# Kernel tuning notes

Hardware: AMD Instinct MI355X
Metric: run time of the kernel (lower is better)

The kernel has to match this reference:

```python
import jax, jax.numpy as jnp
import numpy as np

# model dims
B_, S_, D_ = 2, 2048, 1024
D_STATE, EXPAND, HEADDIM, CHUNK, NGROUPS = 128, 2, 64, 64, 1
D_INNER = EXPAND * D_
NHEADS = D_INNER // HEADDIM  # 32 ssd heads
D_PROJ = 2 * D_INNER + 2 * NGROUPS * D_STATE + NHEADS  # 4384
H_, KV_, HD_ = 16, 4, 64  # attention heads / kv heads / head dim
ROPE_DIMS = 16
MLP_DIM = int(3.0 * D_)


def _rmsnorm(x, w=None, eps=1e-5):
    y = x * jax.lax.rsqrt(jnp.mean(x * x, axis=-1, keepdims=True) + eps)
    return y * w if w is not None else y


def _layernorm(x, w, b, eps=1e-5):
    m = jnp.mean(x, axis=-1, keepdims=True)
    v = jnp.mean((x - m) ** 2, axis=-1, keepdims=True)
    return (x - m) * jax.lax.rsqrt(v + eps) * w + b


def _segsum(x):
    # (..., T) -> (..., T, T) lower-tri cumulative sums, -inf above diag
    T = x.shape[-1]
    i = jnp.arange(T)
    xx = jnp.where(i[:, None] > i[None, :], jnp.broadcast_to(x[..., None], x.shape + (T,)), 0.0)
    s = jnp.cumsum(xx, axis=-2)
    return jnp.where(i[:, None] >= i[None, :], s, -jnp.inf)


def _ssd_chunked(x, A, B, C, chunk):
    # x:(b,s,h,p) A:(b,s,h) B,C:(b,s,g,n)
    b, s, h, p = x.shape
    g, n = B.shape[2], B.shape[3]
    if g < h:
        B = jnp.repeat(B, h // g, axis=2)
        C = jnp.repeat(C, h // g, axis=2)
    c = s // chunk
    x = x.reshape(b, c, chunk, h, p)
    A = A.reshape(b, c, chunk, h).transpose(0, 3, 1, 2)  # b h c l
    B = B.reshape(b, c, chunk, h, n)
    C = C.reshape(b, c, chunk, h, n)
    L = jnp.exp(_segsum(A))
    Y_diag = jnp.einsum('bclhn,bcshn,bhcls,bcshp->bclhp', C, B, L, x)
    A_cum = jnp.cumsum(A, axis=-1)
    decay_states = jnp.exp(A_cum[..., -1:] - A_cum)
    states = jnp.einsum('bclhn,bhcl,bclhp->bchpn', B, decay_states, x)
    decay_chunk = jnp.exp(_segsum(jnp.pad(A_cum[..., -1], ((0, 0), (0, 0), (1, 0)))))
    new_states = jnp.einsum('bhzc,bchpn->bzhpn', decay_chunk[:, :, :c, 1:c + 1], states)
    Y_off = jnp.einsum('bclhn,bchpn,bhcl->bclhp', C, new_states, jnp.exp(A_cum))
    return (Y_diag + Y_off).reshape(b, s, h, p)


def _rope_cos_sin(s, rd, base=10000.0):
    inv = 1.0 / base ** (jnp.arange(0, rd, 2, dtype=jnp.float32) / rd)
    f = jnp.outer(jnp.arange(s, dtype=jnp.float32), inv)  # (s, rd/2)
    return jnp.cos(f)[None, :, None, :], jnp.sin(f)[None, :, None, :]


def _apply_rope(x, cos, sin, rd):
    xr, xp = x[..., :rd], x[..., rd:]
    half = rd // 2
    x1, x2 = xr[..., :half], xr[..., half:]
    xr = jnp.concatenate([x1 * cos + x2 * sin, -x1 * sin + x2 * cos], axis=-1)
    return jnp.concatenate([xr, xp], axis=-1)


def _mamba_block(x, mnorm_w, in_w, out_w, Dp, dt_b, A_log, Bn_w, Cn_w):
    b, s, _ = x.shape
    h = _rmsnorm(x, mnorm_w)
    zxbcdt = h @ in_w.T
    z, xs, Bc, Cc, dt = jnp.split(
        zxbcdt,
        [D_INNER, 2 * D_INNER, 2 * D_INNER + NGROUPS * D_STATE, 2 * D_INNER + 2 * NGROUPS * D_STATE],
        axis=-1)
    dt = jax.nn.softplus(dt + dt_b)  # (b,s,nheads)
    A = -jnp.exp(A_log)  # (nheads,)
    xs = xs.reshape(b, s, NHEADS, HEADDIM)
    Bc = _rmsnorm(Bc.reshape(b, s, NGROUPS, D_STATE), Bn_w)
    Cc = _rmsnorm(Cc.reshape(b, s, NGROUPS, D_STATE), Cn_w)
    y = _ssd_chunked(xs * dt[..., None], A[None, None, :] * dt, Bc, Cc, CHUNK)
    y = y + xs * Dp[None, None, :, None]
    y = y * jax.nn.silu(z).reshape(b, s, NHEADS, HEADDIM)
    return x + y.reshape(b, s, D_INNER) @ out_w.T


def _attn_block(x, ln1_w, ln1_b, cq_w, ck_w, cv_w, cproj_w, q_gain, ln2_w, ln2_b, fc_w, proj_w):
    b, s, d = x.shape
    h = _layernorm(x, ln1_w, ln1_b)
    q = (h @ cq_w.T).reshape(b, s, H_, HD_)
    k = (h @ ck_w.T).reshape(b, s, KV_, HD_)
    v = (h @ cv_w.T).reshape(b, s, KV_, HD_)
    eps = jnp.finfo(x.dtype).eps
    q = _rmsnorm(q, eps=eps)
    k = _rmsnorm(k, eps=eps)
    cos, sin = _rope_cos_sin(s, ROPE_DIMS)
    q = _apply_rope(q, cos, sin, ROPE_DIMS)
    k = _apply_rope(k, cos, sin, ROPE_DIMS)
    q = q * q_gain[None, None, :, None]
    rep = H_ // KV_
    k = jnp.repeat(k, rep, axis=2)
    v = jnp.repeat(v, rep, axis=2)
    scores = jnp.einsum('bqhd,bkhd->bhqk', q, k) / np.float32(np.sqrt(HD_))
    i = jnp.arange(s)
    scores = jnp.where(i[:, None] >= i[None, :], scores, -jnp.inf)
    w = jax.nn.softmax(scores, axis=-1)
    y = jnp.einsum('bhqk,bkhd->bqhd', w, v).reshape(b, s, d)
    x = x + y @ cproj_w.T
    h = _layernorm(x, ln2_w, ln2_b)
    return x + jax.nn.silu(h @ fc_w.T) @ proj_w.T


def setup_inputs() -> dict:
    key = jax.random.key(0)
    ks = jax.random.split(key, 16)
    rn = lambda k, shp, sc=0.02: (jax.random.normal(k, shp, dtype=jnp.float32) * sc)
    return {
        'x': jax.random.normal(ks[0], (B_, S_, D_), dtype=jnp.float32),
        'mnorm_w': jnp.ones((D_,), jnp.float32),
        'in_proj_w': rn(ks[1], (D_PROJ, D_)),
        'out_proj_w': rn(ks[2], (D_, D_INNER)),
        'D_param': jnp.ones((NHEADS,), jnp.float32),
        'dt_bias': rn(ks[3], (NHEADS,), 0.1),
        'A_log': jnp.log(0.5 + jax.random.uniform(ks[4], (NHEADS,), dtype=jnp.float32) * 0.5),
        'Bn_w': jnp.ones((D_STATE,), jnp.float32),
        'Cn_w': jnp.ones((D_STATE,), jnp.float32),
        'ln1_w': jnp.ones((D_,), jnp.float32),
        'ln1_b': jnp.zeros((D_,), jnp.float32),
        'cq_w': rn(ks[5], (D_, D_)),
        'ck_w': rn(ks[6], (KV_ * HD_, D_)),
        'cv_w': rn(ks[7], (KV_ * HD_, D_)),
        'cproj_w': rn(ks[8], (D_, D_)),
        'q_gain': jnp.full((H_,), 5.25, jnp.float32),
        'ln2_w': jnp.ones((D_,), jnp.float32),
        'ln2_b': jnp.zeros((D_,), jnp.float32),
        'fc_w': rn(ks[9], (MLP_DIM, D_)),
        'proj_w': rn(ks[10], (D_, MLP_DIM)),
    }


def reference(x, mnorm_w, in_proj_w, out_proj_w, D_param, dt_bias, A_log, Bn_w, Cn_w,
              ln1_w, ln1_b, cq_w, ck_w, cv_w, cproj_w, q_gain, ln2_w, ln2_b, fc_w, proj_w):
    x = _mamba_block(x, mnorm_w, in_proj_w, out_proj_w, D_param, dt_bias, A_log, Bn_w, Cn_w)
    x = _attn_block(x, ln1_w, ln1_b, cq_w, ck_w, cv_w, cproj_w, q_gain, ln2_w, ln2_b, fc_w, proj_w)
    return x
```

## Files before the change

kernel.cpp:

```cpp
#include <hip/hip_runtime.h>
#include <hip/hip_bf16.h>
#include <math.h>

#define B_    2
#define S_    2048
#define D_    1024
#define DI    2048
#define NH    32
#define HD    64
#define DS    128
#define CH    64
#define NC    32
#define DP    4384
#define HATT  16
#define KVH   4
#define RD    16
#define MLP   3072
#define ROWS  (B_*S_)

typedef __bf16 bf16;
typedef __bf16 bf16x8 __attribute__((ext_vector_type(8)));
typedef __bf16 bf16x4 __attribute__((ext_vector_type(4)));
typedef float  f32x4  __attribute__((ext_vector_type(4)));

__device__ __forceinline__ void async_copy16(const void* g, void* l) {
  __builtin_amdgcn_global_load_lds(
      (const __attribute__((address_space(1))) unsigned int*)g,
      (__attribute__((address_space(3))) unsigned int*)l, 16, 0, 0);
}

__device__ __forceinline__ float waveReduceSum(float v) {
#pragma unroll
  for (int off = 32; off > 0; off >>= 1) v += __shfl_down(v, off, 64);
  return v;
}

template<int NW>
__device__ __forceinline__ float blockReduceSum(float v, float* sh) {
  v = waveReduceSum(v);
  int lane = threadIdx.x & 63, wid = threadIdx.x >> 6;
  if (lane == 0) sh[wid] = v;
  __syncthreads();
  float s = 0.f;
#pragma unroll
  for (int i = 0; i < NW; i++) s += sh[i];
  __syncthreads();
  return s;
}

struct CastSeg { const float* src; bf16* dst; int nval; int ntot; int blk0; };
struct CastArgs { CastSeg seg[8]; };

__global__ __launch_bounds__(256) void castw_all(CastArgs a) {
  int blk = blockIdx.x;
  int si = 0;
#pragma unroll
  for (int i = 1; i < 8; i++) if (blk >= a.seg[i].blk0) si = i;
  CastSeg s = a.seg[si];
  int i = ((blk - s.blk0) * 256 + threadIdx.x) * 4;
  if (i >= s.ntot) return;
  float4 v = {0.f, 0.f, 0.f, 0.f};
  if (i < s.nval) v = *(const float4*)(s.src + i);
  bf16x4 o;
  o[0] = (bf16)v.x; o[1] = (bf16)v.y; o[2] = (bf16)v.z; o[3] = (bf16)v.w;
  *(bf16x4*)(s.dst + i) = o;
}

__global__ __launch_bounds__(256) void rmsnorm_k(const float* __restrict__ x,
                                                 const float* __restrict__ w,
                                                 bf16* __restrict__ y, int n) {
  __shared__ float sh[4];
  size_t row = blockIdx.x;
  const float* xr = x + row * n;
  bf16* yr = y + row * n;
  float ss = 0.f;
  for (int i = threadIdx.x; i < n; i += 256) { float v = xr[i]; ss += v * v; }
  ss = blockReduceSum<4>(ss, sh);
  float inv = rsqrtf(ss / n + 1e-5f);
  for (int i = threadIdx.x; i < n; i += 256) yr[i] = (bf16)(xr[i] * inv * w[i]);
}

template<int ACT, typename OT>
__global__ __launch_bounds__(256) void gemm_mfma(const bf16* __restrict__ A,
                                                 const bf16* __restrict__ W,
                                                 const float* __restrict__ R,
                                                 OT* __restrict__ C,
                                                 int M, int N, int K) {
  __shared__ bf16 As[128 * 32];
  __shared__ bf16 Ws[128 * 32];
  int tid = threadIdx.x, lane = tid & 63, wave = tid >> 6;
  int mt = M >> 7;
  int bid = blockIdx.x;
  int bm = (bid % mt) * 128, bn = (bid / mt) * 128;
  const bf16* gA0 = A + (size_t)(bm + wave * 32 + (lane >> 2)) * K + (lane & 3) * 8;
  const bf16* gA1 = gA0 + (size_t)16 * K;
  const bf16* gW0 = W + (size_t)(bn + wave * 32 + (lane >> 2)) * K + (lane & 3) * 8;
  const bf16* gW1 = gW0 + (size_t)16 * K;
  bf16* lA0 = As + wave * 32 * 32;
  bf16* lA1 = lA0 + 16 * 32;
  bf16* lW0 = Ws + wave * 32 * 32;
  bf16* lW1 = lW0 + 16 * 32;
  int fr = lane & 15, fq = lane >> 4;
  int wm = wave >> 1, wn = wave & 1;
  const bf16* pA = As + (wm * 64 + fr) * 32 + fq * 8;
  const bf16* pW = Ws + (wn * 64 + fr) * 32 + fq * 8;
  f32x4 acc[4][4] = {};
  for (int k0 = 0; k0 < K; k0 += 32) {
    async_copy16(gA0, lA0);
    async_copy16(gA1, lA1);
    async_copy16(gW0, lW0);
    async_copy16(gW1, lW1);
    gA0 += 32; gA1 += 32; gW0 += 32; gW1 += 32;
    __syncthreads();
    bf16x8 af[4], bfr[4];
#pragma unroll
    for (int mi = 0; mi < 4; mi++) af[mi] = *(const bf16x8*)(pA + mi * 16 * 32);
#pragma unroll
    for (int ni = 0; ni < 4; ni++) bfr[ni] = *(const bf16x8*)(pW + ni * 16 * 32);
#pragma unroll
    for (int mi = 0; mi < 4; mi++)
#pragma unroll
      for (int ni = 0; ni < 4; ni++)
        acc[mi][ni] = __builtin_amdgcn_mfma_f32_16x16x32_bf16(af[mi], bfr[ni], acc[mi][ni], 0, 0, 0);
    __syncthreads();
  }
#pragma unroll
  for (int mi = 0; mi < 4; mi++) {
    int row = bm + wm * 64 + mi * 16 + fq * 4;
#pragma unroll
    for (int ni = 0; ni < 4; ni++) {
      int col = bn + wn * 64 + ni * 16 + fr;
      if (col < N) {
#pragma unroll
        for (int r = 0; r < 4; r++) {
          float v = acc[mi][ni][r];
          if (ACT == 1) v = v / (1.f + __expf(-v));
          if (R) v += R[(size_t)(row + r) * N + col];
          C[(size_t)(row + r) * N + col] = (OT)v;
        }
      }
    }
  }
}

__global__ __launch_bounds__(256) void gemm_sk(const bf16* __restrict__ A,
                                               const bf16* __restrict__ W,
                                               bf16* __restrict__ P,
                                               int M, int N, int K, int kchunk) {
  __shared__ bf16 As[128 * 32];
  __shared__ bf16 Ws[128 * 32];
  int tid = threadIdx.x, lane = tid & 63, wave = tid >> 6;
  int mt = M >> 7;
  int bid = blockIdx.x;
  int bm = (bid % mt) * 128, bn = (bid / mt) * 128;
  int ks = blockIdx.z;
  int kbeg = ks * kchunk;
  const bf16* gA0 = A + (size_t)(bm + wave * 32 + (lane >> 2)) * K + kbeg + (lane & 3) * 8;
  const bf16* gA1 = gA0 + (size_t)16 * K;
  const bf16* gW0 = W + (size_t)(bn + wave * 32 + (lane >> 2)) * K + kbeg + (lane & 3) * 8;
  const bf16* gW1 = gW0 + (size_t)16 * K;
  bf16* lA0 = As + wave * 32 * 32;
  bf16* lA1 = lA0 + 16 * 32;
  bf16* lW0 = Ws + wave * 32 * 32;
  bf16* lW1 = lW0 + 16 * 32;
  int fr = lane & 15, fq = lane >> 4;
  int wm = wave >> 1, wn = wave & 1;
  const bf16* pA = As + (wm * 64 + fr) * 32 + fq * 8;
  const bf16* pW = Ws + (wn * 64 + fr) * 32 + fq * 8;
  f32x4 acc[4][4] = {};
  for (int k0 = 0; k0 < kchunk; k0 += 32) {
    async_copy16(gA0, lA0);
    async_copy16(gA1, lA1);
    async_copy16(gW0, lW0);
    async_copy16(gW1, lW1);
    gA0 += 32; gA1 += 32; gW0 += 32; gW1 += 32;
    __syncthreads();
    bf16x8 af[4], bfr[4];
#pragma unroll
    for (int mi = 0; mi < 4; mi++) af[mi] = *(const bf16x8*)(pA + mi * 16 * 32);
#pragma unroll
    for (int ni = 0; ni < 4; ni++) bfr[ni] = *(const bf16x8*)(pW + ni * 16 * 32);
#pragma unroll
    for (int mi = 0; mi < 4; mi++)
#pragma unroll
      for (int ni = 0; ni < 4; ni++)
        acc[mi][ni] = __builtin_amdgcn_mfma_f32_16x16x32_bf16(af[mi], bfr[ni], acc[mi][ni], 0, 0, 0);
    __syncthreads();
  }
  bf16* Pp = P + (size_t)ks * M * N;
#pragma unroll
  for (int mi = 0; mi < 4; mi++) {
    int row = bm + wm * 64 + mi * 16 + fq * 4;
#pragma unroll
    for (int ni = 0; ni < 4; ni++) {
      int col = bn + wn * 64 + ni * 16 + fr;
#pragma unroll
      for (int r = 0; r < 4; r++)
        Pp[(size_t)(row + r) * N + col] = (bf16)acc[mi][ni][r];
    }
  }
}

__global__ __launch_bounds__(256) void reduce_ln2(const bf16* __restrict__ p0,
                                                  const bf16* __restrict__ p1,
                                                  const float* __restrict__ res,
                                                  const float* __restrict__ w,
                                                  const float* __restrict__ b,
                                                  float* __restrict__ xo,
                                                  bf16* __restrict__ ho) {
  __shared__ float sh[4];
  size_t o = (size_t)blockIdx.x * 1024;
  int i = threadIdx.x * 4;
  bf16x4 a = *(const bf16x4*)(p0 + o + i);
  bf16x4 c = *(const bf16x4*)(p1 + o + i);
  f32x4 rv = *(const f32x4*)(res + o + i);
  f32x4 v;
  float s = 0.f, s2 = 0.f;
#pragma unroll
  for (int j = 0; j < 4; j++) {
    v[j] = (float)a[j] + (float)c[j] + rv[j];
    s += v[j]; s2 += v[j] * v[j];
  }
  s  = blockReduceSum<4>(s,  sh);
  s2 = blockReduceSum<4>(s2, sh);
  float mean = s / 1024.f;
  float var  = s2 / 1024.f - mean * mean;
  float inv  = rsqrtf(var + 1e-5f);
  f32x4 wv = *(const f32x4*)(w + i);
  f32x4 bv = *(const f32x4*)(b + i);
  *(f32x4*)(xo + o + i) = v;
  bf16x4 hv;
#pragma unroll
  for (int j = 0; j < 4; j++) hv[j] = (bf16)((v[j] - mean) * inv * wv[j] + bv[j]);
  *(bf16x4*)(ho + o + i) = hv;
}

__global__ __launch_bounds__(256) void reduce_out3(const bf16* __restrict__ p0,
                                                   const bf16* __restrict__ p1,
                                                   const bf16* __restrict__ p2,
                                                   const float* __restrict__ res,
                                                   float* __restrict__ out) {
  int i = (blockIdx.x * 256 + threadIdx.x) * 4;
  bf16x4 a = *(const bf16x4*)(p0 + i);
  bf16x4 c = *(const bf16x4*)(p1 + i);
  bf16x4 d = *(const bf16x4*)(p2 + i);
  f32x4 v = *(const f32x4*)(res + i);
#pragma unroll
  for (int j = 0; j < 4; j++) v[j] += (float)a[j] + (float)c[j] + (float)d[j];
  *(f32x4*)(out + i) = v;
}

__global__ __launch_bounds__(256) void reduce_qkv(const bf16* __restrict__ P,
                                                  const float* __restrict__ q_gain,
                                                  bf16* __restrict__ q,
                                                  bf16* __restrict__ k,
                                                  bf16* __restrict__ v) {
  __shared__ float buf[1536];
  size_t row = blockIdx.x;
  size_t o = row * 1536;
  const bf16* p0 = P + o;
  const bf16* p1 = P + (size_t)ROWS * 1536 + o;
  int tid = threadIdx.x;
  for (int i = tid; i < 384; i += 256) {
    bf16x4 a = *(const bf16x4*)(p0 + i * 4);
    bf16x4 c = *(const bf16x4*)(p1 + i * 4);
    f32x4 vv;
#pragma unroll
    for (int j = 0; j < 4; j++) vv[j] = (float)a[j] + (float)c[j];
    *(f32x4*)(buf + i * 4) = vv;
  }
  __syncthreads();
  int lane = tid & 63, w = tid >> 6;
  int s = (int)(row & (S_ - 1));
  int ri = lane & 7;
  float rinv = __expf(-(float)ri * (0.125f * 9.210340371976184f));
  float ang = (float)s * rinv;
  float cs = cosf(ang), sn = sinf(ang);
#pragma unroll
  for (int j = 0; j < 6; j++) {
    int hh = w * 6 + j;
    float val = buf[hh * 64 + lane];
    if (hh < 20) {
      float ss = val * val;
#pragma unroll
      for (int off = 32; off > 0; off >>= 1) ss += __shfl_xor(ss, off, 64);
      val *= rsqrtf(ss / 64.f + 1.1920929e-7f);
      float other = __shfl_xor(val, 8, 64);
      float res = val;
      if (lane < RD) res = (lane < 8) ? (val * cs + other * sn) : (val * cs - other * sn);
      if (hh < 16) {
        res *= q_gain[hh];
        q[row * (HATT * HD) + hh * HD + lane] = (bf16)res;
      } else {
        k[row * (KVH * HD) + (hh - 16) * HD + lane] = (bf16)res;
      }
    } else {
      v[row * (KVH * HD) + (hh - 20) * HD + lane] = (bf16)val;
    }
  }
}

__global__ __launch_bounds__(512, 2) void gemm256_inproj(const bf16* __restrict__ A,
                                                         const bf16* __restrict__ W,
                                                         bf16* __restrict__ zt,
                                                         bf16* __restrict__ xt,
                                                         bf16* __restrict__ bcdt) {
  __shared__ bf16 lds[3 * 16384];
  int tid = threadIdx.x;
  int lane = tid & 63, w = tid >> 6;
  int fr = lane & 15, fq = lane >> 4;
  int rdswz = (fq ^ (fr & 3)) * 8;
  int sswz = (lane & 3) ^ ((lane >> 2) & 3);
  int bid = blockIdx.x;
  if (bid < 256) {
    int sb = (bid & 7) * 32 + (bid >> 3);
    int bm = (sb & 15) * 256;
    int bn = (sb >> 4) * 256;
    int wm = w >> 2, wn = w & 3;
    int srow = w * 32 + (lane >> 2);
    const bf16* gA = A + (size_t)(bm + srow) * 1024 + sswz * 8;
    const bf16* gW = W + (size_t)(bn + srow) * 1024 + sswz * 8;
    int sbase = w * 1024;
    f32x4 acc[8][4] = {};
    {
      bf16* bA = lds + sbase;
      bf16* bB = lds + 8192 + sbase;
      async_copy16(gA, bA);
      async_copy16(gA + 16 * 1024, bA + 512);
      async_copy16(gW, bB);
      async_copy16(gW + 16 * 1024, bB + 512);
    }
    int cur = 0, nxt = 1;
    for (int t = 0; t < 32; t++) {
      if (t + 1 < 32) {
        const bf16* ga = gA + (t + 1) * 32;
        const bf16* gw = gW + (t + 1) * 32;
        bf16* bA = lds + nxt * 16384 + sbase;
        bf16* bB = lds + nxt * 16384 + 8192 + sbase;
        async_copy16(ga, bA);
        async_copy16(ga + 16 * 1024, bA + 512);
        async_copy16(gw, bB);
        async_copy16(gw + 16 * 1024, bB + 512);
        asm volatile("s_waitcnt vmcnt(4)" ::: "memory");
      } else {
        asm volatile("s_waitcnt vmcnt(0)" ::: "memory");
      }
      __builtin_amdgcn_sched_barrier(0);
      __builtin_amdgcn_s_barrier();
      __builtin_amdgcn_sched_barrier(0);
      const bf16* cA = lds + cur * 16384;
      const bf16* cB = cA + 8192;
      bf16x8 af[8], bfv[4];
#pragma unroll
      for (int mi = 0; mi < 8; mi++)
        af[mi] = *(const bf16x8*)(cA + (wm * 128 + mi * 16 + fr) * 32 + rdswz);
#pragma unroll
      for (int ni = 0; ni < 4; ni++)
        bfv[ni] = *(const bf16x8*)(cB + (wn * 64 + ni * 16 + fr) * 32 + rdswz);
      __builtin_amdgcn_s_setprio(1);
#pragma unroll
      for (int mi = 0; mi < 8; mi++)
#pragma unroll
        for (int ni = 0; ni < 4; ni++)
          acc[mi][ni] = __builtin_amdgcn_mfma_f32_16x16x32_bf16(af[mi], bfv[ni], acc[mi][ni], 0, 0, 0);
      __builtin_amdgcn_s_setprio(0);
      cur = nxt; nxt = nxt + 1; if (nxt == 3) nxt = 0;
    }
    bf16* base = (bn < 2048) ? zt : xt;
    int bq = bm >> 11, bmS = bm & 2047;
    bf16* Ts = lds;
#pragma unroll 1
    for (int g = 0; g < 4; g++) {
      __syncthreads();
      if (wn == g) {
#pragma unroll
        for (int mi = 0; mi < 8; mi++)
#pragma unroll
          for (int ni = 0; ni < 4; ni++) {
            bf16x4 o;
#pragma unroll
            for (int r = 0; r < 4; r++) o[r] = (bf16)acc[mi][ni][r];
            *(bf16x4*)(Ts + (ni * 16 + fr) * 264 + wm * 128 + mi * 16 + fq * 4) = o;
          }
      }
      __syncthreads();
      int hh = ((bn & 2047) + g * 64) >> 6;
      bf16* dst = base + ((size_t)(bq * NH + hh) * HD) * S_ + bmS;
#pragma unroll
      for (int i = 0; i < 4; i++) {
        int idx = tid + i * 512;
        int p = idx >> 5, sc = (idx & 31) * 8;
        *(bf16x8*)(dst + (size_t)p * S_ + sc) = *(const bf16x8*)(Ts + p * 264 + sc);
      }
    }
  } else {
    int lb = bid - 256;
    int bm = (lb & 31) * 128;
    int bn = 4096 + (lb >> 5) * 128;
    int wm = w >> 1, wn = w & 1;
    int srow = w * 16 + (lane >> 2);
    const bf16* gA = A + (size_t)(bm + srow) * 1024 + sswz * 8;
    const bf16* gW = W + (size_t)(bn + srow) * 1024 + sswz * 8;
    int sbase = w * 512;
    f32x4 acc[2][4] = {};
    {
      async_copy16(gA, lds + sbase);
      async_copy16(gW, lds + 4096 + sbase);
    }
    int cur = 0, nxt = 1;
    for (int t = 0; t < 32; t++) {
      if (t + 1 < 32) {
        const bf16* ga = gA + (t + 1) * 32;
        const bf16* gw = gW + (t + 1) * 32;
        async_copy16(ga, lds + nxt * 8192 + sbase);
        async_copy16(gw, lds + nxt * 8192 + 4096 + sbase);
        asm volatile("s_waitcnt vmcnt(2)" ::: "memory");
      } else {
        asm volatile("s_waitcnt vmcnt(0)" ::: "memory");
      }
      __builtin_amdgcn_sched_barrier(0);
      __builtin_amdgcn_s_barrier();
      __builtin_amdgcn_sched_barrier(0);
      const bf16* cA = lds + cur * 8192;
      const bf16* cB = cA + 4096;
      bf16x8 af[2], bfv[4];
#pragma unroll
      for (int mi = 0; mi < 2; mi++)
        af[mi] = *(const bf16x8*)(cA + (wm * 32 + mi * 16 + fr) * 32 + rdswz);
#pragma unroll
      for (int ni = 0; ni < 4; ni++)
        bfv[ni] = *(const bf16x8*)(cB + (wn * 64 + ni * 16 + fr) * 32 + rdswz);
#pragma unroll
      for (int mi = 0; mi < 2; mi++)
#pragma unroll
        for (int ni = 0; ni < 4; ni++)
          acc[mi][ni] = __builtin_amdgcn_mfma_f32_16x16x32_bf16(af[mi], bfv[ni], acc[mi][ni], 0, 0, 0);
      cur = nxt; nxt = nxt + 1; if (nxt == 3) nxt = 0;
    }
#pragma unroll
    for (int mi = 0; mi < 2; mi++) {
      int row = bm + wm * 32 + mi * 16 + fq * 4;
#pragma unroll
      for (int ni = 0; ni < 4; ni++) {
        int col = bn + wn * 64 + ni * 16 + fr;
        if (col < 4384) {
#pragma unroll
          for (int r = 0; r < 4; r++)
            bcdt[(size_t)(row + r) * 288 + (col - 4096)] = (bf16)acc[mi][ni][r];
        }
      }
    }
  }
}

__global__ __launch_bounds__(256) void t64(const bf16* __restrict__ in, bf16* __restrict__ out,
                                           int istr, size_t io, size_t oo, int n_nt) {
  __shared__ bf16 T[64 * 72];
  int bid = blockIdx.x;
  int st = bid & 31;
  int nt = (bid >> 5) % n_nt;
  int outer = bid / (32 * n_nt);
  const bf16* ip = in + outer * io + (size_t)st * 64 * istr + nt * 64;
  int tid = threadIdx.x;
#pragma unroll
  for (int i = 0; i < 2; i++) {
    int cid = tid + i * 256; int s = cid >> 3, pc = (cid & 7) * 8;
    *(bf16x8*)(T + s * 72 + pc) = *(const bf16x8*)(ip + (size_t)s * istr + pc);
  }
  __syncthreads();
  bf16* op = out + outer * oo + (size_t)nt * 64 * 2048 + st * 64;
#pragma unroll
  for (int i = 0; i < 2; i++) {
    int cid = tid + i * 256; int p = cid >> 3, sc = (cid & 7) * 8;
    bf16x8 o;
#pragma unroll
    for (int j = 0; j < 8; j++) o[j] = T[(sc + j) * 72 + p];
    *(bf16x8*)(op + (size_t)p * 2048 + sc) = o;
  }
}

__global__ __launch_bounds__(64) void ssd_prep(const bf16* __restrict__ bcdt,
                                               const float* __restrict__ dt_bias,
                                               const float* __restrict__ A_log,
                                               float* __restrict__ dt_c,
                                               float* __restrict__ ddc,
                                               float* __restrict__ ac_c,
                                               float* __restrict__ T_out) {
  int bid = blockIdx.x;
  int c = bid % NC, hh = (bid / NC) % NH, b = bid / (NC * NH);
  int l = threadIdx.x;
  size_t row = (size_t)b * S_ + c * 64 + l;
  float raw = (float)bcdt[row * 288 + 256 + hh] + dt_bias[hh];
  float dtv = (raw > 20.f) ? raw : log1pf(__expf(raw));
  float a = -__expf(A_log[hh]) * dtv;
  float ps = a;
#pragma unroll
  for (int off = 1; off < 64; off <<= 1) {
    float t = __shfl_up(ps, off, 64);
    if (l >= off) ps += t;
  }
  float a63 = __shfl(ps, 63, 64);
  size_t o = ((size_t)b * NH + hh) * S_ + c * 64 + l;
  dt_c[o] = dtv;
  ac_c[o] = ps;
  ddc[o] = __expf(a63 - ps) * dtv;
  if (l == 63) T_out[(b * NH + hh) * NC + c] = ps;
}

__global__ __launch_bounds__(128) void bc_norm(const bf16* __restrict__ bcdt,
                                               const float* __restrict__ Bw,
                                               const float* __restrict__ Cw,
                                               bf16* __restrict__ Bn,
                                               bf16* __restrict__ Cn) {
  __shared__ float shb[2], shc[2];
  size_t row = blockIdx.x;
  int i = threadIdx.x;
  float bv = (float)bcdt[row * 288 + i];
  float cv = (float)bcdt[row * 288 + 128 + i];
  float sb = waveReduceSum(bv * bv);
  float sc = waveReduceSum(cv * cv);
  int lane = threadIdx.x & 63, wid = threadIdx.x >> 6;
  if (lane == 0) { shb[wid] = sb; shc[wid] = sc; }
  __syncthreads();
  float tb = shb[0] + shb[1];
  float tc = shc[0] + shc[1];
  Bn[row * DS + i] = (bf16)(bv * rsqrtf(tb / DS + 1e-5f) * Bw[i]);
  Cn[row * DS + i] = (bf16)(cv * rsqrtf(tc / DS + 1e-5f) * Cw[i]);
}

__global__ __launch_bounds__(256) void ssd_states(const bf16* __restrict__ Xt,
                                                  const bf16* __restrict__ Btr,
                                                  const float* __restrict__ ddc,
                                                  bf16* __restrict__ states) {
  __shared__ bf16 Xs[64 * 72];
  __shared__ bf16 Bs[128 * 72];
  int bid = blockIdx.x;
  int h = bid % NH;
  int c = (bid / NH) % NC;
  int b = bid / (NH * NC);
  int tid = threadIdx.x, lane = tid & 63, w = tid >> 6;
  int fr = lane & 15, fq = lane >> 4;
  const size_t xbase = (size_t)(b * NH + h) * HD * S_ + c * 64;
  const size_t dbase = (size_t)(b * NH + h) * S_ + c * 64;
#pragma unroll
  for (int i = 0; i < 2; i++) {
    int cid = tid + i * 256; int p = cid >> 3, sc = (cid & 7) * 8;
    bf16x8 xv = *(const bf16x8*)(Xt + xbase + (size_t)p * S_ + sc);
    f32x4 d0 = *(const f32x4*)(ddc + dbase + sc);
    f32x4 d1 = *(const f32x4*)(ddc + dbase + sc + 4);
    bf16x8 o;
#pragma unroll
    for (int j = 0; j < 4; j++) { o[j] = (bf16)((float)xv[j] * d0[j]); o[4 + j] = (bf16)((float)xv[4 + j] * d1[j]); }
    *(bf16x8*)(Xs + p * 72 + sc) = o;
  }
  const size_t bbase = (size_t)b * 128 * S_ + c * 64;
#pragma unroll
  for (int i = 0; i < 4; i++) {
    int cid = tid + i * 256; int n = cid >> 3, sc = (cid & 7) * 8;
    *(bf16x8*)(Bs + n * 72 + sc) = *(const bf16x8*)(Btr + bbase + (size_t)n * S_ + sc);
  }
  __syncthreads();
  f32x4 acc[4][2] = {};
#pragma unroll
  for (int ks = 0; ks < 2; ks++) {
    bf16x8 a[4], bb[2];
#pragma unroll
    for (int pt = 0; pt < 4; pt++) a[pt] = *(const bf16x8*)(Xs + (pt * 16 + fr) * 72 + ks * 32 + fq * 8);
#pragma unroll
    for (int n2 = 0; n2 < 2; n2++) bb[n2] = *(const bf16x8*)(Bs + ((2 * w + n2) * 16 + fr) * 72 + ks * 32 + fq * 8);
#pragma unroll
    for (int pt = 0; pt < 4; pt++)
#pragma unroll
      for (int n2 = 0; n2 < 2; n2++)
        acc[pt][n2] = __builtin_amdgcn_mfma_f32_16x16x32_bf16(a[pt], bb[n2], acc[pt][n2], 0, 0, 0);
  }
  bf16* outp = states + (size_t)bid * 8192;
#pragma unroll
  for (int pt = 0; pt < 4; pt++)
#pragma unroll
    for (int n2 = 0; n2 < 2; n2++) {
      int n = (2 * w + n2) * 16 + fr;
#pragma unroll
      for (int r = 0; r < 4; r++)
        outp[(size_t)(pt * 16 + fq * 4 + r) * 128 + n] = (bf16)acc[pt][n2][r];
    }
}

__global__ __launch_bounds__(256) void ssd_scan(bf16* __restrict__ states,
                                                const float* __restrict__ T) {
  __shared__ float eT[NC];
  int part = blockIdx.x & 7;
  int bh = blockIdx.x >> 3;
  int b = bh / NH, h = bh % NH;
  if (threadIdx.x < NC) eT[threadIdx.x] = __expf(T[(size_t)(b * NH + h) * NC + threadIdx.x]);
  __syncthreads();
  const size_t cstride = (size_t)NH * HD * DS;
  size_t base = ((size_t)b * NC * NH + h) * (HD * DS);
#pragma unroll
  for (int j = 0; j < 4; j++) {
    int e = part * 1024 + threadIdx.x + j * 256;
    float carry = 0.f;
    size_t idx = base + e;
    for (int c = 0; c < NC; c++) {
      float sv = (float)states[idx];
      states[idx] = (bf16)carry;
      carry = sv + eT[c] * carry;
      idx += cstride;
    }
  }
}

__global__ __launch_bounds__(256) void ssd_out(const bf16* __restrict__ Cn,
                                               const bf16* __restrict__ Bn,
                                               const bf16* __restrict__ Xt,
                                               const bf16* __restrict__ Zt,
                                               const float* __restrict__ dt_c,
                                               const float* __restrict__ ac_c,
                                               const bf16* __restrict__ states,
                                               const float* __restrict__ Dp,
                                               bf16* __restrict__ ybf) {
  __shared__ bf16 Cs[64 * 136];
  __shared__ bf16 BNs[64 * 136];
  __shared__ bf16 Xs[64 * 72];
  __shared__ bf16 G[64 * 72];
  __shared__ float acs[64];
  int bid = blockIdx.x;
  int h = bid % NH;
  int c = (bid / NH) % NC;
  int b = bid / (NH * NC);
  int tid = threadIdx.x, lane = tid & 63, w = tid >> 6;
  int fr = lane & 15, fq = lane >> 4;
  size_t row0 = (size_t)b * S_ + c * 64;
  const size_t abase = (size_t)(b * NH + h) * S_ + c * 64;
  if (tid < 64) acs[tid] = ac_c[abase + tid];
#pragma unroll
  for (int i = 0; i < 4; i++) {
    int cid = tid + i * 256; int l = cid >> 4, nc = (cid & 15) * 8;
    float e = __expf(ac_c[abase + l]);
    bf16x8 cv = *(const bf16x8*)(Cn + (row0 + l) * DS + nc);
    bf16x8 o;
#pragma unroll
    for (int j = 0; j < 8; j++) o[j] = (bf16)((float)cv[j] * e);
    *(bf16x8*)(Cs + l * 136 + nc) = o;
    *(bf16x8*)(BNs + l * 136 + nc) = *(const bf16x8*)(Bn + (row0 + l) * DS + nc);
  }
  const size_t xbase = (size_t)(b * NH + h) * HD * S_ + c * 64;
#pragma unroll
  for (int i = 0; i < 2; i++) {
    int cid = tid + i * 256; int p = cid >> 3, sc = (cid & 7) * 8;
    bf16x8 xv = *(const bf16x8*)(Xt + xbase + (size_t)p * S_ + sc);
    f32x4 d0 = *(const f32x4*)(dt_c + abase + sc);
    f32x4 d1 = *(const f32x4*)(dt_c + abase + sc + 4);
    bf16x8 o;
#pragma unroll
    for (int j = 0; j < 4; j++) { o[j] = (bf16)((float)xv[j] * d0[j]); o[4 + j] = (bf16)((float)xv[4 + j] * d1[j]); }
    *(bf16x8*)(Xs + p * 72 + sc) = o;
  }
  __syncthreads();
  bf16x8 ca[4];
#pragma unroll
  for (int ks = 0; ks < 4; ks++) ca[ks] = *(const bf16x8*)(Cs + (w * 16 + fr) * 136 + ks * 32 + fq * 8);
  f32x4 cb[4] = {};
  for (int st = 0; st <= w; st++)
#pragma unroll
    for (int ks = 0; ks < 4; ks++)
      cb[st] = __builtin_amdgcn_mfma_f32_16x16x32_bf16(ca[ks],
                 *(const bf16x8*)(BNs + (st * 16 + fr) * 136 + ks * 32 + fq * 8), cb[st], 0, 0, 0);
#pragma unroll
  for (int st = 0; st < 4; st++) {
    float es = (st <= w) ? __expf(-acs[st * 16 + fr]) : 0.f;
#pragma unroll
    for (int r = 0; r < 4; r++) {
      int lloc = fq * 4 + r;
      float g = 0.f;
      if (st < w) g = cb[st][r] * es;
      else if (st == w) g = (lloc >= fr) ? cb[st][r] * es : 0.f;
      G[(w * 16 + lloc) * 72 + st * 16 + fr] = (bf16)g;
    }
  }
  f32x4 acc[4] = {};
  {
    bf16x8 ga0 = *(const bf16x8*)(G + (w * 16 + fr) * 72 + fq * 8);
    bf16x8 ga1 = *(const bf16x8*)(G + (w * 16 + fr) * 72 + 32 + fq * 8);
#pragma unroll
    for (int pt = 0; pt < 4; pt++) {
      acc[pt] = __builtin_amdgcn_mfma_f32_16x16x32_bf16(ga0,
                  *(const bf16x8*)(Xs + (pt * 16 + fr) * 72 + fq * 8), acc[pt], 0, 0, 0);
      acc[pt] = __builtin_amdgcn_mfma_f32_16x16x32_bf16(ga1,
                  *(const bf16x8*)(Xs + (pt * 16 + fr) * 72 + 32 + fq * 8), acc[pt], 0, 0, 0);
    }
  }
  __syncthreads();
  const bf16* stp = states + (size_t)bid * 8192;
#pragma unroll
  for (int i = 0; i < 4; i++) {
    int cid = tid + i * 256; int p = cid >> 4, nc = (cid & 15) * 8;
    *(bf16x8*)(BNs + p * 136 + nc) = *(const bf16x8*)(stp + (size_t)p * 128 + nc);
  }
  __syncthreads();
#pragma unroll
  for (int pt = 0; pt < 4; pt++)
#pragma unroll
    for (int ks = 0; ks < 4; ks++)
      acc[pt] = __builtin_amdgcn_mfma_f32_16x16x32_bf16(ca[ks],
                  *(const bf16x8*)(BNs + (pt * 16 + fr) * 136 + ks * 32 + fq * 8), acc[pt], 0, 0, 0);
  float dph = Dp[h];
#pragma unroll
  for (int pt = 0; pt < 4; pt++) {
    int p = pt * 16 + fr;
    size_t tb = (xbase + (size_t)p * S_) + w * 16 + fq * 4;
    bf16x4 xs4 = *(const bf16x4*)(Xt + tb);
    bf16x4 z4  = *(const bf16x4*)(Zt + tb);
#pragma unroll
    for (int r = 0; r < 4; r++) {
      int l = w * 16 + fq * 4 + r;
      float yv = acc[pt][r] + (float)xs4[r] * dph;
      float z = (float)z4[r];
      yv *= z / (1.f + __expf(-z));
      ybf[((row0 + l) * NH + h) * HD + p] = (bf16)yv;
    }
  }
}

#define KSTR 72
#define PSTR 72
__global__ __launch_bounds__(256) void attn_mfma(const bf16* __restrict__ q,
                                                 const bf16* __restrict__ k,
                                                 const bf16* __restrict__ vtr,
                                                 bf16* __restrict__ Po,
                                                 float* __restrict__ Ls) {
  __shared__ bf16 Ks[64 * KSTR];
  __shared__ bf16 Vs[64 * KSTR];
  __shared__ bf16 Pl[4][32 * PSTR];
  int c = 39 - blockIdx.x;
  int g = (c < 4) ? 0 : (c < 12) ? 1 : (c < 24) ? 2 : 3;
  int gbase = (g == 0) ? 0 : (g == 1) ? 4 : (g == 2) ? 12 : 24;
  int d = c - gbase;
  int qt = 4 * g + d / (g + 1);
  int sk = d % (g + 1);
  int h = blockIdx.y, b = blockIdx.z;
  int kvh = h >> 2;
  int tid = threadIdx.x, lane = tid & 63, w = tid >> 6;
  int fr = lane & 15, fq = lane >> 4;
  const float SC = 0.18033688011112042f;
  const float M2 = 62.0f;
  int kt0 = sk * 8;
  int ktend = min(kt0 + 8, 2 * qt + 2);
  int qbase = qt * 128 + w * 32;
  int qmaxw = qbase + 31;
  bf16x8 bq[2][2];
#pragma unroll
  for (int qc = 0; qc < 2; qc++)
#pragma unroll
    for (int ks = 0; ks < 2; ks++)
      bq[qc][ks] = *(const bf16x8*)(q + (size_t)(b * S_ + qbase + qc * 16 + fr) * (HATT * HD)
                                      + h * HD + ks * 32 + fq * 8);
  int sr = tid >> 3, sc8 = (tid & 7) * 8;
  const bf16* kg = k + ((size_t)(b * S_) + sr) * (KVH * HD) + kvh * HD + sc8;
  const bf16* vg = vtr + ((size_t)(b * KVH + kvh) * HD + sr) * S_ + sc8;
  bf16x8 krg0, krg1, vrg0, vrg1;
  {
    const bf16* kp = kg + (size_t)kt0 * 64 * (KVH * HD);
    const bf16* vp = vg + (size_t)kt0 * 64;
    krg0 = *(const bf16x8*)(kp);
    krg1 = *(const bf16x8*)(kp + (size_t)32 * (KVH * HD));
    vrg0 = *(const bf16x8*)(vp);
    vrg1 = *(const bf16x8*)(vp + (size_t)32 * S_);
  }
  float lsum[2] = {0.f, 0.f};
  f32x4 yacc[2][4] = {};
  bf16* Plw = Pl[w];
  for (int kt = kt0; kt < ktend; kt++) {
    __syncthreads();
    *(bf16x8*)(&Ks[sr * KSTR + sc8]) = krg0;
    *(bf16x8*)(&Ks[(sr + 32) * KSTR + sc8]) = krg1;
    *(bf16x8*)(&Vs[sr * KSTR + sc8]) = vrg0;
    *(bf16x8*)(&Vs[(sr + 32) * KSTR + sc8]) = vrg1;
    __syncthreads();
    if ((kt + 1) < ktend) {
      const bf16* kp = kg + (size_t)(kt + 1) * 64 * (KVH * HD);
      const bf16* vp = vg + (size_t)(kt + 1) * 64;
      krg0 = *(const bf16x8*)(kp);
      krg1 = *(const bf16x8*)(kp + (size_t)32 * (KVH * HD));
      vrg0 = *(const bf16x8*)(vp);
      vrg1 = *(const bf16x8*)(vp + (size_t)32 * S_);
    }
    if (kt * 64 <= qmaxw) {
      bool nomask = (kt * 64 + 63) <= qbase;
      if (nomask) {
#pragma unroll
        for (int mi = 0; mi < 4; mi++) {
          const bf16* krow = &Ks[(mi * 16 + fr) * KSTR];
          bf16x8 ak0 = *(const bf16x8*)(krow + fq * 8);
          bf16x8 ak1 = *(const bf16x8*)(krow + 32 + fq * 8);
#pragma unroll
          for (int qc = 0; qc < 2; qc++) {
            f32x4 s = {};
            s = __builtin_amdgcn_mfma_f32_16x16x32_bf16(ak0, bq[qc][0], s, 0, 0, 0);
            s = __builtin_amdgcn_mfma_f32_16x16x32_bf16(ak1, bq[qc][1], s, 0, 0, 0);
            bf16x4 pk;
#pragma unroll
            for (int r = 0; r < 4; r++) {
              float p = __builtin_amdgcn_exp2f(s[r] * SC - M2);
              lsum[qc] += p;
              pk[r] = (bf16)p;
            }
            *(bf16x4*)(Plw + (qc * 16 + fr) * PSTR + mi * 16 + fq * 4) = pk;
          }
        }
      } else {
#pragma unroll
        for (int mi = 0; mi < 4; mi++) {
          int s0 = kt * 64 + mi * 16;
          if (s0 > qmaxw) {
            bf16x4 zz = {};
#pragma unroll
            for (int qc = 0; qc < 2; qc++)
              *(bf16x4*)(Plw + (qc * 16 + fr) * PSTR + mi * 16 + fq * 4) = zz;
          } else {
            const bf16* krow = &Ks[(mi * 16 + fr) * KSTR];
            bf16x8 ak0 = *(const bf16x8*)(krow + fq * 8);
            bf16x8 ak1 = *(const bf16x8*)(krow + 32 + fq * 8);
#pragma unroll
            for (int qc = 0; qc < 2; qc++) {
              f32x4 s = {};
              s = __builtin_amdgcn_mfma_f32_16x16x32_bf16(ak0, bq[qc][0], s, 0, 0, 0);
              s = __builtin_amdgcn_mfma_f32_16x16x32_bf16(ak1, bq[qc][1], s, 0, 0, 0);
              int qq = qbase + qc * 16 + fr;
              bf16x4 pk;
#pragma unroll
              for (int r = 0; r < 4; r++) {
                int sp = s0 + fq * 4 + r;
                float p = (sp <= qq) ? __builtin_amdgcn_exp2f(s[r] * SC - M2) : 0.f;
                lsum[qc] += p;
                pk[r] = (bf16)p;
              }
              *(bf16x4*)(Plw + (qc * 16 + fr) * PSTR + mi * 16 + fq * 4) = pk;
            }
          }
        }
      }
#pragma unroll
      for (int ks2 = 0; ks2 < 2; ks2++) {
        bf16x8 bp[2];
#pragma unroll
        for (int qc = 0; qc < 2; qc++)
          bp[qc] = *(const bf16x8*)(Plw + (qc * 16 + fr) * PSTR + ks2 * 32 + fq * 8);
#pragma unroll
        for (int pi = 0; pi < 4; pi++) {
          bf16x8 av = *(const bf16x8*)(&Vs[(pi * 16 + fr) * KSTR + ks2 * 32 + fq * 8]);
#pragma unroll
          for (int qc = 0; qc < 2; qc++)
            yacc[qc][pi] = __builtin_amdgcn_mfma_f32_16x16x32_bf16(av, bp[qc], yacc[qc][pi], 0, 0, 0);
        }
      }
    }
  }
#pragma unroll
  for (int qc = 0; qc < 2; qc++) {
    lsum[qc] += __shfl_xor(lsum[qc], 16, 64);
    lsum[qc] += __shfl_xor(lsum[qc], 32, 64);
    int qrow = qt * 128 + w * 32 + qc * 16 + fr;
    if (fq == 0)
      Ls[((size_t)(b * 16 + h) * 2048 + qrow) * 4 + sk] = lsum[qc];
    bf16* pop = Po + ((((size_t)(b * 16 + h) * 16 + qt) * 4 + sk) * 128
                       + w * 32 + qc * 16 + fr) * 64 + fq * 4;
#pragma unroll
    for (int pi = 0; pi < 4; pi++) {
      bf16x4 o;
#pragma unroll
      for (int r = 0; r < 4; r++) o[r] = (bf16)yacc[qc][pi][r];
      *(bf16x4*)(pop + pi * 16) = o;
    }
  }
}

__global__ __launch_bounds__(256) void attn_red(const bf16* __restrict__ Po,
                                                const float* __restrict__ Ls,
                                                bf16* __restrict__ y2) {
  int row = blockIdx.x;
  int b = row >> 11;
  int qrow = row & 2047;
  int qt = qrow >> 7, r = qrow & 127;
  int nch = (qt >> 2) + 1;
  int t = threadIdx.x;
  int h = t >> 4, e4 = (t & 15) << 2;
  const float* lp = Ls + ((size_t)(b * 16 + h) * 2048 + qrow) * 4;
  float ls = 0.f;
  f32x4 acc = {};
  for (int sk = 0; sk < nch; sk++) {
    ls += lp[sk];
    const bf16* pp = Po + ((((size_t)(b * 16 + h) * 16 + qt) * 4 + sk) * 128 + r) * 64 + e4;
    bf16x4 v = *(const bf16x4*)(pp);
#pragma unroll
    for (int j = 0; j < 4; j++) acc[j] += (float)v[j];
  }
  float inv = 1.f / ls;
  bf16x4 o;
#pragma unroll
  for (int j = 0; j < 4; j++) o[j] = (bf16)(acc[j] * inv);
  *(bf16x4*)(y2 + (size_t)row * 1024 + h * 64 + e4) = o;
}

constexpr size_t OFF_WIN  = 0;
constexpr size_t OFF_WOUT = 9175040;
constexpr size_t OFF_WQKV = 13369344;
constexpr size_t OFF_WCP  = 16515072;
constexpr size_t OFF_WFC  = 18612224;
constexpr size_t OFF_WPR  = 24903680;
constexpr size_t OFF_HBF  = 31195136;
constexpr size_t OFF_BCDT = 39583744;
constexpr size_t OFF_XT   = 41943040;
constexpr size_t OFF_ZT   = 58720256;
constexpr size_t OFF_DTC  = 75497472;
constexpr size_t OFF_DDC  = 76546048;
constexpr size_t OFF_ACC  = 77594624;
constexpr size_t OFF_T    = 78643200;
constexpr size_t OFF_BN   = 78651392;
constexpr size_t OFF_CN   = 79699968;
constexpr size_t OFF_BTR  = 80748544;
constexpr size_t OFF_ST   = 81797120;
constexpr size_t OFF_YBF  = 148905984;
constexpr size_t OFF_X1   = 165683200;
constexpr size_t OFF_P    = OFF_ST;
constexpr size_t OFF_PO   = OFF_ST;
constexpr size_t OFF_LS   = OFF_BCDT;
constexpr size_t OFF_QB   = OFF_XT;
constexpr size_t OFF_KB   = OFF_XT + 8388608;
constexpr size_t OFF_VB   = OFF_XT + 10485760;
constexpr size_t OFF_VTR  = OFF_XT + 12582912;
constexpr size_t OFF_Y2   = OFF_ZT;
constexpr size_t OFF_X2   = 50331648;
constexpr size_t OFF_MLP  = 132128768;

extern "C" void kernel_launch(void* const* d_in, const int* in_sizes, int n_in,
                              void* d_out, int out_size, void* d_ws, size_t ws_size,
                              hipStream_t stream) {
  (void)in_sizes; (void)n_in; (void)out_size; (void)ws_size;
  const float* x        = (const float*)d_in[0];
  const float* mnorm_w  = (const float*)d_in[1];
  const float* in_w     = (const float*)d_in[2];
  const float* out_w    = (const float*)d_in[3];
  const float* Dp       = (const float*)d_in[4];
  const float* dt_bias  = (const float*)d_in[5];
  const float* A_log    = (const float*)d_in[6];
  const float* Bn_w     = (const float*)d_in[7];
  const float* Cn_w     = (const float*)d_in[8];
  const float* ln1_w    = (const float*)d_in[9];
  const float* ln1_b    = (const float*)d_in[10];
  const float* cq_w     = (const float*)d_in[11];
  const float* ck_w     = (const float*)d_in[12];
  const float* cv_w     = (const float*)d_in[13];
  const float* cproj_w  = (const float*)d_in[14];
  const float* q_gain   = (const float*)d_in[15];
  const float* ln2_w    = (const float*)d_in[16];
  const float* ln2_b    = (const float*)d_in[17];
  const float* fc_w     = (const float*)d_in[18];
  const float* proj_w   = (const float*)d_in[19];
  float* out = (float*)d_out;
  char* W8 = (char*)d_ws;

  bf16* w_in   = (bf16*)(W8 + OFF_WIN);
  bf16* w_out  = (bf16*)(W8 + OFF_WOUT);
  bf16* w_qkv  = (bf16*)(W8 + OFF_WQKV);
  bf16* w_cp   = (bf16*)(W8 + OFF_WCP);
  bf16* w_fc   = (bf16*)(W8 + OFF_WFC);
  bf16* w_pr   = (bf16*)(W8 + OFF_WPR);
  bf16* h_bf   = (bf16*)(W8 + OFF_HBF);
  bf16* bcdt   = (bf16*)(W8 + OFF_BCDT);
  bf16* Xt     = (bf16*)(W8 + OFF_XT);
  bf16* Zt     = (bf16*)(W8 + OFF_ZT);
  float* dt_c  = (float*)(W8 + OFF_DTC);
  float* ddc   = (float*)(W8 + OFF_DDC);
  float* ac_c  = (float*)(W8 + OFF_ACC);
  float* Tb    = (float*)(W8 + OFF_T);
  bf16* Bn     = (bf16*)(W8 + OFF_BN);
  bf16* Cn     = (bf16*)(W8 + OFF_CN);
  bf16* Btr    = (bf16*)(W8 + OFF_BTR);
  bf16* st     = (bf16*)(W8 + OFF_ST);
  bf16* ybf    = (bf16*)(W8 + OFF_YBF);
  float* x1    = (float*)(W8 + OFF_X1);
  bf16* Pbuf   = (bf16*)(W8 + OFF_P);
  bf16* Po     = (bf16*)(W8 + OFF_PO);
  float* Ls    = (float*)(W8 + OFF_LS);
  bf16* qbf    = (bf16*)(W8 + OFF_QB);
  bf16* kbf    = (bf16*)(W8 + OFF_KB);
  bf16* vbf    = (bf16*)(W8 + OFF_VB);
  bf16* vtr    = (bf16*)(W8 + OFF_VTR);
  bf16* y2     = (bf16*)(W8 + OFF_Y2);
  float* x2    = (float*)(W8 + OFF_X2);
  bf16* mlp    = (bf16*)(W8 + OFF_MLP);

  CastArgs ca;
  ca.seg[0] = { in_w,    w_in,            4489216, 4587520, 0     };
  ca.seg[1] = { out_w,   w_out,           2097152, 2097152, 4480  };
  ca.seg[2] = { cq_w,    w_qkv,           1048576, 1048576, 6528  };
  ca.seg[3] = { ck_w,    w_qkv + 1048576,  262144,  262144, 7552  };
  ca.seg[4] = { cv_w,    w_qkv + 1310720,  262144,  262144, 7808  };
  ca.seg[5] = { cproj_w, w_cp,            1048576, 1048576, 8064  };
  ca.seg[6] = { fc_w,    w_fc,            3145728, 3145728, 9088  };
  ca.seg[7] = { proj_w,  w_pr,            3145728, 3145728, 12160 };
  castw_all<<<15232, 256, 0, stream>>>(ca);

  const size_t PS  = (size_t)ROWS * 1024;

  rmsnorm_k<<<ROWS, 256, 0, stream>>>(x, mnorm_w, h_bf, D_);
  gemm256_inproj<<<352, 512, 0, stream>>>(h_bf, w_in, Zt, Xt, bcdt);
  ssd_prep<<<B_ * NH * NC, 64, 0, stream>>>(bcdt, dt_bias, A_log, dt_c, ddc, ac_c, Tb);
  bc_norm<<<ROWS, 128, 0, stream>>>(bcdt, Bn_w, Cn_w, Bn, Cn);
  t64<<<2 * 2 * 32, 256, 0, stream>>>(Bn, Btr, 128, (size_t)2048 * 128, (size_t)128 * 2048, 2);
  ssd_states<<<B_ * NC * NH, 256, 0, stream>>>(Xt, Btr, ddc, st);
  ssd_scan<<<B_ * NH * 8, 256, 0, stream>>>(st, Tb);
  ssd_out<<<B_ * NC * NH, 256, 0, stream>>>(Cn, Bn, Xt, Zt, dt_c, ac_c, st, Dp, ybf);
  gemm_sk<<<dim3(32 * 8, 1, 2), 256, 0, stream>>>(ybf, w_out, Pbuf, ROWS, D_, DI, 1024);
  reduce_ln2<<<ROWS, 256, 0, stream>>>(Pbuf, Pbuf + PS, x, ln1_w, ln1_b, x1, h_bf);

  gemm_sk<<<dim3(32 * 12, 1, 2), 256, 0, stream>>>(h_bf, w_qkv, Pbuf, ROWS, 1536, D_, 512);
  reduce_qkv<<<ROWS, 256, 0, stream>>>(Pbuf, q_gain, qbf, kbf, vbf);
  t64<<<2 * 4 * 32, 256, 0, stream>>>(vbf, vtr, 256, (size_t)2048 * 256, (size_t)256 * 2048, 4);
  attn_mfma<<<dim3(40, HATT, B_), 256, 0, stream>>>(qbf, kbf, vtr, Po, Ls);
  attn_red<<<ROWS, 256, 0, stream>>>(Po, Ls, y2);
  gemm_sk<<<dim3(32 * 8, 1, 2), 256, 0, stream>>>(y2, w_cp, Pbuf, ROWS, D_, D_, 512);
  reduce_ln2<<<ROWS, 256, 0, stream>>>(Pbuf, Pbuf + PS, x1, ln2_w, ln2_b, x2, h_bf);

  gemm_mfma<1, bf16><<<32 * 24, 256, 0, stream>>>(h_bf, w_fc, nullptr, mlp, ROWS, MLP, D_);
  gemm_sk<<<dim3(32 * 8, 1, 3), 256, 0, stream>>>(mlp, w_pr, Pbuf, ROWS, D_, MLP, 1024);
  reduce_out3<<<ROWS, 256, 0, stream>>>(Pbuf, Pbuf + PS, Pbuf + 2 * PS, x2, out);
}
```

Baseline: 510.9 us.

## Triple-buffer LDS tiles in MFMA GEMMs with async prefetch and single barrier

Both GEMM kernels now use a three-stage LDS ring. The next k-tile's global-to-LDS async copies are issued before computing on the current tile, and vmcnt waits replace the two __syncthreads per iteration with one barrier. This aims to overlap global load latency with MFMA work, and s_setprio raises wave priority around the MFMA block. LDS use grows from 16KB to 48KB per block, which may reduce occupancy, and the correctness of the single-barrier ring depends on the three-buffer distance.

```diff
diff --git a/kernel.cpp b/kernel.cpp
--- a/kernel.cpp
+++ b/kernel.cpp
@@ -86,8 +86,7 @@
                                                  const float* __restrict__ R,
                                                  OT* __restrict__ C,
                                                  int M, int N, int K) {
-  __shared__ bf16 As[128 * 32];
-  __shared__ bf16 Ws[128 * 32];
+  __shared__ bf16 lds[3 * 8192];
   int tid = threadIdx.x, lane = tid & 63, wave = tid >> 6;
   int mt = M >> 7;
   int bid = blockIdx.x;
@@ -96,33 +95,49 @@
   const bf16* gA1 = gA0 + (size_t)16 * K;
   const bf16* gW0 = W + (size_t)(bn + wave * 32 + (lane >> 2)) * K + (lane & 3) * 8;
   const bf16* gW1 = gW0 + (size_t)16 * K;
-  bf16* lA0 = As + wave * 32 * 32;
-  bf16* lA1 = lA0 + 16 * 32;
-  bf16* lW0 = Ws + wave * 32 * 32;
-  bf16* lW1 = lW0 + 16 * 32;
+  int sA = wave * 1024;
   int fr = lane & 15, fq = lane >> 4;
   int wm = wave >> 1, wn = wave & 1;
-  const bf16* pA = As + (wm * 64 + fr) * 32 + fq * 8;
-  const bf16* pW = Ws + (wn * 64 + fr) * 32 + fq * 8;
+  int rdA = (wm * 64 + fr) * 32 + fq * 8;
+  int rdW = (wn * 64 + fr) * 32 + fq * 8;
   f32x4 acc[4][4] = {};
-  for (int k0 = 0; k0 < K; k0 += 32) {
-    async_copy16(gA0, lA0);
-    async_copy16(gA1, lA1);
-    async_copy16(gW0, lW0);
-    async_copy16(gW1, lW1);
-    gA0 += 32; gA1 += 32; gW0 += 32; gW1 += 32;
-    __syncthreads();
+  {
+    bf16* bA = lds + sA;
+    bf16* bW = lds + 4096 + sA;
+    async_copy16(gA0, bA);  async_copy16(gA1, bA + 512);
+    async_copy16(gW0, bW);  async_copy16(gW1, bW + 512);
+  }
+  int cur = 0, nxt = 1;
+  int nsteps = K >> 5;
+  for (int t = 0; t < nsteps; t++) {
+    if (t + 1 < nsteps) {
+      int off = (t + 1) * 32;
+      bf16* bA = lds + nxt * 8192 + sA;
+      bf16* bW = lds + nxt * 8192 + 4096 + sA;
+      async_copy16(gA0 + off, bA);  async_copy16(gA1 + off, bA + 512);
+      async_copy16(gW0 + off, bW);  async_copy16(gW1 + off, bW + 512);
+      asm volatile("s_waitcnt vmcnt(4)" ::: "memory");
+    } else {
+      asm volatile("s_waitcnt vmcnt(0)" ::: "memory");
+    }
+    __builtin_amdgcn_sched_barrier(0);
+    __builtin_amdgcn_s_barrier();
+    __builtin_amdgcn_sched_barrier(0);
+    const bf16* cA = lds + cur * 8192;
+    const bf16* cW = cA + 4096;
     bf16x8 af[4], bfr[4];
 #pragma unroll
-    for (int mi = 0; mi < 4; mi++) af[mi] = *(const bf16x8*)(pA + mi * 16 * 32);
-#pragma unroll
-    for (int ni = 0; ni < 4; ni++) bfr[ni] = *(const bf16x8*)(pW + ni * 16 * 32);
+    for (int mi = 0; mi < 4; mi++) af[mi] = *(const bf16x8*)(cA + rdA + mi * 512);
+#pragma unroll
+    for (int ni = 0; ni < 4; ni++) bfr[ni] = *(const bf16x8*)(cW + rdW + ni * 512);
+    __builtin_amdgcn_s_setprio(1);
 #pragma unroll
     for (int mi = 0; mi < 4; mi++)
 #pragma unroll
       for (int ni = 0; ni < 4; ni++)
         acc[mi][ni] = __builtin_amdgcn_mfma_f32_16x16x32_bf16(af[mi], bfr[ni], acc[mi][ni], 0, 0, 0);
-    __syncthreads();
+    __builtin_amdgcn_s_setprio(0);
+    cur = nxt; nxt = nxt + 1; if (nxt == 3) nxt = 0;
   }
 #pragma unroll
   for (int mi = 0; mi < 4; mi++) {
@@ -147,8 +162,7 @@
                                                const bf16* __restrict__ W,
                                                bf16* __restrict__ P,
                                                int M, int N, int K, int kchunk) {
-  __shared__ bf16 As[128 * 32];
-  __shared__ bf16 Ws[128 * 32];
+  __shared__ bf16 lds[3 * 8192];
   int tid = threadIdx.x, lane = tid & 63, wave = tid >> 6;
   int mt = M >> 7;
   int bid = blockIdx.x;
@@ -159,33 +173,49 @@
   const bf16* gA1 = gA0 + (size_t)16 * K;
   const bf16* gW0 = W + (size_t)(bn + wave * 32 + (lane >> 2)) * K + kbeg + (lane & 3) * 8;
   const bf16* gW1 = gW0 + (size_t)16 * K;
-  bf16* lA0 = As + wave * 32 * 32;
-  bf16* lA1 = lA0 + 16 * 32;
-  bf16* lW0 = Ws + wave * 32 * 32;
-  bf16* lW1 = lW0 + 16 * 32;
+  int sA = wave * 1024;
   int fr = lane & 15, fq = lane >> 4;
   int wm = wave >> 1, wn = wave & 1;
-  const bf16* pA = As + (wm * 64 + fr) * 32 + fq * 8;
-  const bf16* pW = Ws + (wn * 64 + fr) * 32 + fq * 8;
+  int rdA = (wm * 64 + fr) * 32 + fq * 8;
+  int rdW = (wn * 64 + fr) * 32 + fq * 8;
   f32x4 acc[4][4] = {};
-  for (int k0 = 0; k0 < kchunk; k0 += 32) {
-    async_copy16(gA0, lA0);
-    async_copy16(gA1, lA1);
-    async_copy16(gW0, lW0);
-    async_copy16(gW1, lW1);
-    gA0 += 32; gA1 += 32; gW0 += 32; gW1 += 32;
-    __syncthreads();
+  {
+    bf16* bA = lds + sA;
+    bf16* bW = lds + 4096 + sA;
+    async_copy16(gA0, bA);  async_copy16(gA1, bA + 512);
+    async_copy16(gW0, bW);  async_copy16(gW1, bW + 512);
+  }
+  int cur = 0, nxt = 1;
+  int nsteps = kchunk >> 5;
+  for (int t = 0; t < nsteps; t++) {
+    if (t + 1 < nsteps) {
+      int off = (t + 1) * 32;
+      bf16* bA = lds + nxt * 8192 + sA;
+      bf16* bW = lds + nxt * 8192 + 4096 + sA;
+      async_copy16(gA0 + off, bA);  async_copy16(gA1 + off, bA + 512);
+      async_copy16(gW0 + off, bW);  async_copy16(gW1 + off, bW + 512);
+      asm volatile("s_waitcnt vmcnt(4)" ::: "memory");
+    } else {
+      asm volatile("s_waitcnt vmcnt(0)" ::: "memory");
+    }
+    __builtin_amdgcn_sched_barrier(0);
+    __builtin_amdgcn_s_barrier();
+    __builtin_amdgcn_sched_barrier(0);
+    const bf16* cA = lds + cur * 8192;
+    const bf16* cW = cA + 4096;
     bf16x8 af[4], bfr[4];
 #pragma unroll
-    for (int mi = 0; mi < 4; mi++) af[mi] = *(const bf16x8*)(pA + mi * 16 * 32);
-#pragma unroll
-    for (int ni = 0; ni < 4; ni++) bfr[ni] = *(const bf16x8*)(pW + ni * 16 * 32);
+    for (int mi = 0; mi < 4; mi++) af[mi] = *(const bf16x8*)(cA + rdA + mi * 512);
+#pragma unroll
+    for (int ni = 0; ni < 4; ni++) bfr[ni] = *(const bf16x8*)(cW + rdW + ni * 512);
+    __builtin_amdgcn_s_setprio(1);
 #pragma unroll
     for (int mi = 0; mi < 4; mi++)
 #pragma unroll
       for (int ni = 0; ni < 4; ni++)
         acc[mi][ni] = __builtin_amdgcn_mfma_f32_16x16x32_bf16(af[mi], bfr[ni], acc[mi][ni], 0, 0, 0);
-    __syncthreads();
+    __builtin_amdgcn_s_setprio(0);
+    cur = nxt; nxt = nxt + 1; if (nxt == 3) nxt = 0;
   }
   bf16* Pp = P + (size_t)ks * M * N;
 #pragma unroll
```

After: 499.3 us. 2.3% less time.
